# Performance work log

Hardware: AMD Instinct MI355X
Metric: run time of the kernel (lower is better)

Reference implementation:

```python
import jax, jax.numpy as jnp
import numpy as np

D_MODEL = 1024
NUM_HEADS = 16
D_K = D_MODEL // NUM_HEADS
THETA = 10000.0
BATCH, SEQ = 2, 2048


def _rope(xh, pos):
    # xh: (..., h, s, d_k), pos: (s,) int
    half = D_K // 2
    inv_freq = THETA ** (-jnp.arange(half, dtype=jnp.float32) * 2.0 / D_K)  # (half,)
    ang = pos.astype(jnp.float32)[:, None] * inv_freq[None, :]              # (s, half)
    cos, sin = jnp.cos(ang), jnp.sin(ang)
    x1 = xh[..., 0::2]  # (..., h, s, half)
    x2 = xh[..., 1::2]
    r1 = x1 * cos - x2 * sin
    r2 = x1 * sin + x2 * cos
    out = jnp.stack([r1, r2], axis=-1)            # (..., h, s, half, 2)
    return out.reshape(xh.shape)


def setup_inputs() -> dict:
    key = jax.random.key(0)
    k1, k2, k3 = jax.random.split(key, 3)
    scale_qkv = (6.0 / (3 * D_MODEL + D_MODEL)) ** 0.5  # xavier uniform bound
    scale_o = (6.0 / (2 * D_MODEL)) ** 0.5
    return {
        "x": jax.random.normal(k1, (BATCH, SEQ, D_MODEL), dtype=jnp.float32),
        "token_positions": jnp.arange(SEQ, dtype=jnp.int64 if jax.config.jax_enable_x64 else jnp.int32),
        "qkv_proj": jax.random.uniform(k2, (3 * D_MODEL, D_MODEL), jnp.float32, -scale_qkv, scale_qkv),
        "o_proj": jax.random.uniform(k3, (D_MODEL, D_MODEL), jnp.float32, -scale_o, scale_o),
    }


def reference(x, token_positions, qkv_proj, o_proj):
    # fused QKV projection: x @ qkv_proj^T
    qkv = jnp.einsum('bsd,ed->bse', x, qkv_proj)          # (b, s, 3*d_model)
    q, k, v = jnp.split(qkv, 3, axis=-1)

    def to_heads(t):
        b, s, _ = t.shape
        return t.reshape(b, s, NUM_HEADS, D_K).transpose(0, 2, 1, 3)  # (b, h, s, d_k)

    qh, kh, vh = to_heads(q), to_heads(k), to_heads(v)
    qh = _rope(qh, token_positions)
    kh = _rope(kh, token_positions)

    scores = jnp.einsum('bhqd,bhkd->bhqk', qh, kh) / (D_K ** 0.5)
    s = x.shape[-2]
    causal = jnp.tril(jnp.ones((s, s), dtype=bool))
    scores = jnp.where(causal, scores, -jnp.inf)
    attn = jax.nn.softmax(scores, axis=-1)
    out = jnp.einsum('bhqk,bhkd->bhqd', attn, vh)          # (b, h, s, d_k)
    out = out.transpose(0, 2, 1, 3).reshape(x.shape[0], s, D_MODEL)
    return jnp.einsum('bsd,od->bso', out, o_proj)
```

## Files before the change

### kernel.cpp

```cpp
#include <hip/hip_runtime.h>
#include <hip/hip_bf16.h>
#include <math.h>

typedef __bf16 bf16_t;
typedef __attribute__((ext_vector_type(2))) __bf16 bf16x2;
typedef __attribute__((ext_vector_type(4))) __bf16 bf16x4;
typedef __attribute__((ext_vector_type(8))) __bf16 bf16x8;
typedef __attribute__((ext_vector_type(4))) float f32x4;

#define BATCH  2
#define SEQ    2048
#define DMODEL 1024
#define NHEADS 16
#define DK     64

typedef const __attribute__((address_space(1))) void* gas_t;
typedef __attribute__((address_space(3))) void* las_t;

#define X_N (BATCH * SEQ * DMODEL)
#define W_N (3 * DMODEL * DMODEL)
#define O_N (DMODEL * DMODEL)

__global__ __launch_bounds__(256) void convert_kernel(
    const float* __restrict__ x, const float* __restrict__ w, const float* __restrict__ o,
    bf16_t* __restrict__ xb, bf16_t* __restrict__ wb, bf16_t* __restrict__ ob)
{
    const int gid = blockIdx.x * 256 + threadIdx.x;
    const float* src; bf16_t* dst; int base = gid * 8;
    if (base < X_N)                { src = x; dst = xb; }
    else if (base < X_N + W_N)     { src = w; dst = wb; base -= X_N; }
    else                           { src = o; dst = ob; base -= X_N + W_N; }
    const f32x4 lo = *(const f32x4*)(src + base);
    const f32x4 hi = *(const f32x4*)(src + base + 4);
    bf16x8 r;
    r[0] = (bf16_t)lo[0]; r[1] = (bf16_t)lo[1]; r[2] = (bf16_t)lo[2]; r[3] = (bf16_t)lo[3];
    r[4] = (bf16_t)hi[0]; r[5] = (bf16_t)hi[1]; r[6] = (bf16_t)hi[2]; r[7] = (bf16_t)hi[3];
    *(bf16x8*)(dst + base) = r;
}

__device__ __forceinline__ void gemm128_body(
    const bf16_t* __restrict__ A, const bf16_t* __restrict__ B,
    int rowBase, int colBase, bf16_t* ldsA, bf16_t* ldsB, f32x4 acc[4][4])
{
    const int tid  = threadIdx.x;
    const int lane = tid & 63;
    const int l15  = lane & 15, quad = lane >> 4;
    const int qr   = ((tid >> 6) >> 1) * 64;
    const int qc   = ((tid >> 6) & 1) * 64;

    const int c0 = tid, c1 = tid + 256;
    const int r0 = c0 >> 2, kc0 = (c0 & 3) * 8;
    const int r1 = c1 >> 2, kc1 = (c1 & 3) * 8;
    const bf16_t* ga0 = A + (size_t)(rowBase + r0) * DMODEL + kc0;
    const bf16_t* ga1 = A + (size_t)(rowBase + r1) * DMODEL + kc1;
    const bf16_t* gb0 = B + (size_t)(colBase + r0) * DMODEL + kc0;
    const bf16_t* gb1 = B + (size_t)(colBase + r1) * DMODEL + kc1;

    for (int k0 = 0; k0 < DMODEL; k0 += 32) {
        __syncthreads();
        __builtin_amdgcn_global_load_lds((gas_t)(ga0 + k0), (las_t)(ldsA + c0 * 8), 16, 0, 0);
        __builtin_amdgcn_global_load_lds((gas_t)(ga1 + k0), (las_t)(ldsA + c1 * 8), 16, 0, 0);
        __builtin_amdgcn_global_load_lds((gas_t)(gb0 + k0), (las_t)(ldsB + c0 * 8), 16, 0, 0);
        __builtin_amdgcn_global_load_lds((gas_t)(gb1 + k0), (las_t)(ldsB + c1 * 8), 16, 0, 0);
        __syncthreads();

        bf16x8 af[4], bfr[4];
#pragma unroll
        for (int i = 0; i < 4; ++i)
            af[i] = *(const bf16x8*)&ldsA[(qr + i * 16 + l15) * 32 + quad * 8];
#pragma unroll
        for (int j = 0; j < 4; ++j)
            bfr[j] = *(const bf16x8*)&ldsB[(qc + j * 16 + l15) * 32 + quad * 8];
#pragma unroll
        for (int i = 0; i < 4; ++i)
#pragma unroll
            for (int j = 0; j < 4; ++j)
                acc[i][j] = __builtin_amdgcn_mfma_f32_16x16x32_bf16(af[i], bfr[j], acc[i][j], 0, 0, 0);
    }
}

__global__ __launch_bounds__(256) void qkv_gemm_kernel(
    const bf16_t* __restrict__ x, const bf16_t* __restrict__ w,
    const int* __restrict__ pos,
    bf16_t* __restrict__ qo, bf16_t* __restrict__ ko, bf16_t* __restrict__ vt)
{
    __shared__ bf16_t ldsA[128 * 32];
    __shared__ bf16_t ldsB[128 * 32];
    const int bid = blockIdx.x;
    const int xcd = bid & 7, t = bid >> 3;
    const int xh  = xcd >> 2, yh = xcd & 3;
    const int bx  = xh * 12 + (t % 12);
    const int by  = yh * 8  + (t / 12);
    const int rowBase = by * 128;
    const int colBase = bx * 128;
    f32x4 acc[4][4] = {};
    gemm128_body(x, w, rowBase, colBase, ldsA, ldsB, acc);

    const int lane = threadIdx.x & 63;
    const int l15 = lane & 15, quad = lane >> 4;
    const int qr = ((threadIdx.x >> 6) >> 1) * 64;
    const int qc = ((threadIdx.x >> 6) & 1) * 64;
#pragma unroll
    for (int j = 0; j < 4; ++j) {
        const int col  = colBase + qc + j * 16 + l15;
        const int part = col >> 10;
        const int h    = (col & 1023) >> 6;
        const int d    = col & 63;
        bf16_t* op = (part == 0) ? qo : (part == 1) ? ko : vt;
        if (part < 2) {
            const float invf  = exp2f(-(float)(d >> 1) * 0.4152410118609203f);
            const float psign = (d & 1) ? 1.f : -1.f;
#pragma unroll
            for (int i = 0; i < 4; ++i) {
#pragma unroll
                for (int r = 0; r < 4; ++r) {
                    const int m = rowBase + qr + i * 16 + quad * 4 + r;
                    const int b = m >> 11;
                    const int s = m & (SEQ - 1);
                    const float ang = (float)pos[s] * invf;
                    const float sn_ = __sinf(ang);
                    const float c_  = __cosf(ang);
                    const float v = acc[i][j][r];
                    const float p = __shfl_xor(v, 1);
                    const float res = fmaf(p, psign * sn_, v * c_);
                    op[((size_t)(b * NHEADS + h) * SEQ + s) * DK + d] = (bf16_t)res;
                }
            }
        } else {
#pragma unroll
            for (int i = 0; i < 4; ++i) {
#pragma unroll
                for (int r = 0; r < 4; ++r) {
                    const int m = rowBase + qr + i * 16 + quad * 4 + r;
                    const int b = m >> 11;
                    const int s = m & (SEQ - 1);
                    const int sp = (s & ~63) | ((s & 15) << 2) | ((s >> 4) & 3);
                    op[(size_t)(b * NHEADS + h) * SEQ * DK + (size_t)d * SEQ + sp]
                        = (bf16_t)acc[i][j][r];
                }
            }
        }
    }
}

__global__ __launch_bounds__(256) void out_gemm_kernel(
    const bf16_t* __restrict__ a, const bf16_t* __restrict__ w, float* __restrict__ out)
{
    __shared__ bf16_t ldsA[2 * 128 * 64];
    __shared__ bf16_t ldsB[2 * 64 * 64];
    const int tid  = threadIdx.x;
    const int lane = tid & 63;
    const int l15  = lane & 15, quad = lane >> 4;
    const int l7   = l15 & 7;
    const int wv   = tid >> 6;
    const int bid = blockIdx.x;
    const int xcd = bid & 7, t = bid >> 3;
    const int xh  = xcd >> 2, yh = xcd & 3;
    const int bx  = xh * 8 + (t & 7);
    const int by  = yh * 8 + (t >> 3);
    const int rowBase = by * 128;
    const int colBase = bx * 64;

    const int sr   = tid >> 3;
    const int scol = ((tid & 7) ^ (sr & 7)) * 8;
    const bf16_t* ga = a + (size_t)(rowBase + sr) * DMODEL + scol;
    const bf16_t* gb = w + (size_t)(colBase + sr) * DMODEL + scol;
    const int dd = tid * 8;

#pragma unroll
    for (int u = 0; u < 4; ++u)
        __builtin_amdgcn_global_load_lds((gas_t)(ga + (size_t)u * 32 * DMODEL),
                                         (las_t)(ldsA + dd + u * 2048), 16, 0, 0);
#pragma unroll
    for (int u = 0; u < 2; ++u)
        __builtin_amdgcn_global_load_lds((gas_t)(gb + (size_t)u * 32 * DMODEL),
                                         (las_t)(ldsB + dd + u * 2048), 16, 0, 0);
    __syncthreads();

    f32x4 acc[2][4] = {};
    int buf = 0;
    for (int k0 = 0; k0 < DMODEL; k0 += 64) {
        if (k0 + 64 < DMODEL) {
            const int offA = (buf ^ 1) * 8192, offB = (buf ^ 1) * 4096;
#pragma unroll
            for (int u = 0; u < 4; ++u)
                __builtin_amdgcn_global_load_lds((gas_t)(ga + k0 + 64 + (size_t)u * 32 * DMODEL),
                                                 (las_t)(ldsA + offA + dd + u * 2048), 16, 0, 0);
#pragma unroll
            for (int u = 0; u < 2; ++u)
                __builtin_amdgcn_global_load_lds((gas_t)(gb + k0 + 64 + (size_t)u * 32 * DMODEL),
                                                 (las_t)(ldsB + offB + dd + u * 2048), 16, 0, 0);
        }
        const bf16_t* La = ldsA + buf * 8192;
        const bf16_t* Lb = ldsB + buf * 4096;
#pragma unroll
        for (int kk = 0; kk < 2; ++kk) {
            const int sw = ((kk * 4 + quad) ^ l7) * 8;
            bf16x8 af[2], bfr[4];
#pragma unroll
            for (int i = 0; i < 2; ++i)
                af[i] = *(const bf16x8*)&La[(wv * 32 + i * 16 + l15) * 64 + sw];
#pragma unroll
            for (int j = 0; j < 4; ++j)
                bfr[j] = *(const bf16x8*)&Lb[(j * 16 + l15) * 64 + sw];
#pragma unroll
            for (int i = 0; i < 2; ++i)
#pragma unroll
                for (int j = 0; j < 4; ++j)
                    acc[i][j] = __builtin_amdgcn_mfma_f32_16x16x32_bf16(af[i], bfr[j], acc[i][j], 0, 0, 0);
        }
        __syncthreads();
        buf ^= 1;
    }
#pragma unroll
    for (int i = 0; i < 2; ++i) {
#pragma unroll
        for (int r = 0; r < 4; ++r) {
            const int m = rowBase + wv * 32 + i * 16 + quad * 4 + r;
#pragma unroll
            for (int j = 0; j < 4; ++j)
                out[(size_t)m * DMODEL + colBase + j * 16 + l15] = acc[i][j][r];
        }
    }
}

__global__ __launch_bounds__(256) void attn_kernel(
    const bf16_t* __restrict__ Q, const bf16_t* __restrict__ K,
    const bf16_t* __restrict__ VT, bf16_t* __restrict__ AO)
{
    __shared__ bf16_t Kb[64 * 64];
    __shared__ bf16_t Vb[64 * 64];
    __shared__ bf16_t Pb[4][16 * 72];

    const int bh = blockIdx.x & 31;
    const int j  = blockIdx.x >> 5;
    const int lo = j & 7, hi = j >> 3;
    const int qb = (hi == 0) ? lo
                 : (hi == 1) ? (31 - lo)
                 : (hi == 2) ? (8 + lo)
                 :             (23 - lo);
    const int nt = qb + 1;

    const int tid  = threadIdx.x;
    const int wave = tid >> 6, lane = tid & 63;
    const int l15  = lane & 15, quad = lane >> 4;
    const int q0   = qb * 64 + wave * 16;
    const size_t hb = (size_t)bh * SEQ * DK;

    const int r0 = tid >> 3;
    const int sc = ((tid & 7) ^ (r0 & 7)) * 8;
    const int dd0 = tid * 8, dd1 = (tid + 256) * 8;

    bf16x8 aq0, aq1;
    {
        const bf16_t* qrow = Q + hb + (size_t)(q0 + l15) * DK + quad * 8;
        aq0 = *(const bf16x8*)qrow;
        aq1 = *(const bf16x8*)(qrow + 32);
#pragma unroll
        for (int i = 0; i < 8; ++i) {
            aq0[i] = (bf16_t)((float)aq0[i] * 0.125f);
            aq1[i] = (bf16_t)((float)aq1[i] * 0.125f);
        }
    }

    f32x4 oacc[4] = {};
    float lsum[4] = {};
    const int swA = (quad ^ (l15 & 7)) * 8;
    const int swB = ((4 + quad) ^ (l15 & 7)) * 8;

    for (int kb = 0; kb < nt; ++kb) {
        __syncthreads();
        {
            const bf16_t* kg = K  + hb + (size_t)kb * 64 * DK + (size_t)r0 * DK  + sc;
            const bf16_t* vg = VT + hb + kb * 64 + (size_t)r0 * SEQ + sc;
            __builtin_amdgcn_global_load_lds((gas_t)kg,              (las_t)(&Kb[dd0]), 16, 0, 0);
            __builtin_amdgcn_global_load_lds((gas_t)(kg + 32 * DK),  (las_t)(&Kb[dd1]), 16, 0, 0);
            __builtin_amdgcn_global_load_lds((gas_t)vg,              (las_t)(&Vb[dd0]), 16, 0, 0);
            __builtin_amdgcn_global_load_lds((gas_t)(vg + 32 * SEQ), (las_t)(&Vb[dd1]), 16, 0, 0);
        }
        __syncthreads();

        const bool nm = (kb == qb);

        bf16x8 kf0[4], kf1[4];
#pragma unroll
        for (int c = 0; c < 4; ++c) {
            kf0[c] = *(const bf16x8*)&Kb[(c * 16 + l15) * 64 + swA];
            kf1[c] = *(const bf16x8*)&Kb[(c * 16 + l15) * 64 + swB];
        }
        f32x4 sc4[4];
#pragma unroll
        for (int c = 0; c < 4; ++c) {
            f32x4 z = {};
            z = __builtin_amdgcn_mfma_f32_16x16x32_bf16(aq0, kf0[c], z, 0, 0, 0);
            z = __builtin_amdgcn_mfma_f32_16x16x32_bf16(aq1, kf1[c], z, 0, 0, 0);
            sc4[c] = z;
        }
#pragma unroll
        for (int r = 0; r < 4; ++r) {
            bf16x4 pr;
#pragma unroll
            for (int c = 0; c < 4; ++c) {
                float s = sc4[c][r];
                if (nm) {
                    const int key = kb * 64 + c * 16 + l15;
                    const int qa  = q0 + quad * 4 + r;
                    s = (key <= qa) ? s : -INFINITY;
                }
                const float p = __expf(s - 8.0f);
                lsum[r] += p;
                pr[c] = (bf16_t)p;
            }
            *(bf16x4*)&Pb[wave][(quad * 4 + r) * 72 + l15 * 4] = pr;
        }
        asm volatile("s_waitcnt lgkmcnt(0)" ::: "memory");

        const bf16x8 ap0 = *(const bf16x8*)&Pb[wave][l15 * 72 + quad * 8];
        const bf16x8 ap1 = *(const bf16x8*)&Pb[wave][l15 * 72 + 32 + quad * 8];
#pragma unroll
        for (int t = 0; t < 4; ++t) {
            const bf16x8 bv0 = *(const bf16x8*)&Vb[(t * 16 + l15) * 64 + swA];
            const bf16x8 bv1 = *(const bf16x8*)&Vb[(t * 16 + l15) * 64 + swB];
            oacc[t] = __builtin_amdgcn_mfma_f32_16x16x32_bf16(ap0, bv0, oacc[t], 0, 0, 0);
            oacc[t] = __builtin_amdgcn_mfma_f32_16x16x32_bf16(ap1, bv1, oacc[t], 0, 0, 0);
        }
    }

    const int b = bh >> 4, h = bh & 15;
    float inv[4];
#pragma unroll
    for (int r = 0; r < 4; ++r) {
        float s = lsum[r];
        s += __shfl_xor(s, 1);
        s += __shfl_xor(s, 2);
        s += __shfl_xor(s, 4);
        s += __shfl_xor(s, 8);
        inv[r] = 1.0f / s;
    }
#pragma unroll
    for (int t = 0; t < 4; ++t)
#pragma unroll
        for (int r = 0; r < 4; ++r) {
            const int qa = q0 + quad * 4 + r;
            AO[(size_t)(b * SEQ + qa) * DMODEL + h * 64 + t * 16 + l15] =
                (bf16_t)(oacc[t][r] * inv[r]);
        }
}

extern "C" void kernel_launch(void* const* d_in, const int* in_sizes, int n_in,
                              void* d_out, int out_size, void* d_ws, size_t ws_size,
                              hipStream_t stream) {
    (void)in_sizes; (void)n_in; (void)out_size; (void)ws_size;
    const float* x    = (const float*)d_in[0];
    const int*   pos  = (const int*)d_in[1];
    const float* qkvw = (const float*)d_in[2];
    const float* ow   = (const float*)d_in[3];
    float* out = (float*)d_out;

    const size_t HEAD_ELEMS = (size_t)BATCH * NHEADS * SEQ * DK;
    bf16_t* Qw  = (bf16_t*)d_ws;
    bf16_t* Kw  = Qw + HEAD_ELEMS;
    bf16_t* Vt  = Kw + HEAD_ELEMS;
    bf16_t* AO  = Vt + HEAD_ELEMS;
    bf16_t* xb  = AO;
    bf16_t* wb  = AO + X_N;
    bf16_t* ob  = wb + W_N;

    convert_kernel<<<dim3(4096), 256, 0, stream>>>(x, qkvw, ow, xb, wb, ob);
    qkv_gemm_kernel<<<dim3(768), 256, 0, stream>>>(xb, wb, pos, Qw, Kw, Vt);
    attn_kernel<<<dim3(1024), 256, 0, stream>>>(Qw, Kw, Vt, AO);
    out_gemm_kernel<<<dim3(512), 256, 0, stream>>>(AO, ob, out);
}
```

Baseline: 183.0 us.

## Rewrite QKV GEMM with 256x192 tiles, double-buffered LDS and swizzle

Replaces the 128x128, k=32, single-buffer QKV GEMM with a 512-thread block computing 256x192 tiles. It uses a 64-wide k step, a double-buffered LDS prefetch with explicit vmcnt waits, an XOR swizzle to avoid LDS bank conflicts, and setprio around the MFMA bursts. Larger tiles raise arithmetic intensity and cut global traffic, and the prefetch overlaps loads with compute. The trade-off is 256 blocks (one wave of CUs), heavy LDS use (~112KB) and more accumulator registers per thread, which lowers occupancy.

```diff
diff --git a/kernel.cpp b/kernel.cpp
--- a/kernel.cpp
+++ b/kernel.cpp
@@ -38,83 +38,105 @@
     *(bf16x8*)(dst + base) = r;
 }
 
-__device__ __forceinline__ void gemm128_body(
-    const bf16_t* __restrict__ A, const bf16_t* __restrict__ B,
-    int rowBase, int colBase, bf16_t* ldsA, bf16_t* ldsB, f32x4 acc[4][4])
-{
-    const int tid  = threadIdx.x;
-    const int lane = tid & 63;
-    const int l15  = lane & 15, quad = lane >> 4;
-    const int qr   = ((tid >> 6) >> 1) * 64;
-    const int qc   = ((tid >> 6) & 1) * 64;
-
-    const int c0 = tid, c1 = tid + 256;
-    const int r0 = c0 >> 2, kc0 = (c0 & 3) * 8;
-    const int r1 = c1 >> 2, kc1 = (c1 & 3) * 8;
-    const bf16_t* ga0 = A + (size_t)(rowBase + r0) * DMODEL + kc0;
-    const bf16_t* ga1 = A + (size_t)(rowBase + r1) * DMODEL + kc1;
-    const bf16_t* gb0 = B + (size_t)(colBase + r0) * DMODEL + kc0;
-    const bf16_t* gb1 = B + (size_t)(colBase + r1) * DMODEL + kc1;
-
-    for (int k0 = 0; k0 < DMODEL; k0 += 32) {
-        __syncthreads();
-        __builtin_amdgcn_global_load_lds((gas_t)(ga0 + k0), (las_t)(ldsA + c0 * 8), 16, 0, 0);
-        __builtin_amdgcn_global_load_lds((gas_t)(ga1 + k0), (las_t)(ldsA + c1 * 8), 16, 0, 0);
-        __builtin_amdgcn_global_load_lds((gas_t)(gb0 + k0), (las_t)(ldsB + c0 * 8), 16, 0, 0);
-        __builtin_amdgcn_global_load_lds((gas_t)(gb1 + k0), (las_t)(ldsB + c1 * 8), 16, 0, 0);
-        __syncthreads();
-
-        bf16x8 af[4], bfr[4];
-#pragma unroll
-        for (int i = 0; i < 4; ++i)
-            af[i] = *(const bf16x8*)&ldsA[(qr + i * 16 + l15) * 32 + quad * 8];
-#pragma unroll
-        for (int j = 0; j < 4; ++j)
-            bfr[j] = *(const bf16x8*)&ldsB[(qc + j * 16 + l15) * 32 + quad * 8];
-#pragma unroll
-        for (int i = 0; i < 4; ++i)
-#pragma unroll
-            for (int j = 0; j < 4; ++j)
-                acc[i][j] = __builtin_amdgcn_mfma_f32_16x16x32_bf16(af[i], bfr[j], acc[i][j], 0, 0, 0);
-    }
-}
-
-__global__ __launch_bounds__(256) void qkv_gemm_kernel(
+__global__ __launch_bounds__(512) void qkv_gemm_kernel(
     const bf16_t* __restrict__ x, const bf16_t* __restrict__ w,
     const int* __restrict__ pos,
     bf16_t* __restrict__ qo, bf16_t* __restrict__ ko, bf16_t* __restrict__ vt)
 {
-    __shared__ bf16_t ldsA[128 * 32];
-    __shared__ bf16_t ldsB[128 * 32];
+    __shared__ bf16_t Abuf[2][256 * 64];
+    __shared__ bf16_t Bbuf[2][192 * 64];
+
+    const int tid  = threadIdx.x;
+    const int lane = tid & 63;
+    const int l15  = lane & 15, quad = lane >> 4;
+    const int l7   = l15 & 7;
+    const int wv   = tid >> 6;
+    const int wr   = wv >> 2;
+    const int wc   = wv & 3;
+
     const int bid = blockIdx.x;
-    const int xcd = bid & 7, t = bid >> 3;
-    const int xh  = xcd >> 2, yh = xcd & 3;
-    const int bx  = xh * 12 + (t % 12);
-    const int by  = yh * 8  + (t / 12);
-    const int rowBase = by * 128;
-    const int colBase = bx * 128;
-    f32x4 acc[4][4] = {};
-    gemm128_body(x, w, rowBase, colBase, ldsA, ldsB, acc);
-
-    const int lane = threadIdx.x & 63;
-    const int l15 = lane & 15, quad = lane >> 4;
-    const int qr = ((threadIdx.x >> 6) >> 1) * 64;
-    const int qc = ((threadIdx.x >> 6) & 1) * 64;
-#pragma unroll
-    for (int j = 0; j < 4; ++j) {
-        const int col  = colBase + qc + j * 16 + l15;
-        const int part = col >> 10;
-        const int h    = (col & 1023) >> 6;
-        const int d    = col & 63;
+    const int xcd = bid & 7, tt = bid >> 3;
+    const int yh  = xcd >> 1, ch = xcd & 1;
+    const int bx  = ch * 8 + (tt & 7);
+    const int by  = yh * 4 + (tt >> 3);
+    const int rowBase = by * 256;
+    const int colBase = bx * 192;
+
+    const int r0   = tid >> 3;
+    const int scol = ((tid & 7) ^ (r0 & 7)) * 8;
+    const bf16_t* Ax = x + (size_t)(rowBase + r0) * DMODEL + scol;
+    const bf16_t* Bx = w + (size_t)(colBase + r0) * DMODEL + scol;
+
+    f32x4 acc[8][3] = {};
+
+#define STAGE(kt, bufi)                                                          \
+    {                                                                            \
+        const int k0_ = (kt) * 64;                                               \
+        _Pragma("unroll")                                                        \
+        for (int l = 0; l < 4; ++l)                                              \
+            __builtin_amdgcn_global_load_lds(                                    \
+                (gas_t)(Ax + (size_t)(l * 64) * DMODEL + k0_),                   \
+                (las_t)(&Abuf[bufi][(l * 512 + tid) * 8]), 16, 0, 0);            \
+        _Pragma("unroll")                                                        \
+        for (int l = 0; l < 3; ++l)                                              \
+            __builtin_amdgcn_global_load_lds(                                    \
+                (gas_t)(Bx + (size_t)(l * 64) * DMODEL + k0_),                   \
+                (las_t)(&Bbuf[bufi][(l * 512 + tid) * 8]), 16, 0, 0);            \
+    }
+
+    STAGE(0, 0)
+    STAGE(1, 1)
+    asm volatile("s_waitcnt vmcnt(7)" ::: "memory");
+    __builtin_amdgcn_s_barrier();
+    __builtin_amdgcn_sched_barrier(0);
+
+    for (int t = 0; t < 16; ++t) {
+        const int buf = t & 1;
+#pragma unroll
+        for (int kk = 0; kk < 2; ++kk) {
+            const int sw = ((kk * 4 + quad) ^ l7) * 8;
+            bf16x8 bfr[3];
+#pragma unroll
+            for (int j = 0; j < 3; ++j)
+                bfr[j] = *(const bf16x8*)&Bbuf[buf][(wc * 48 + j * 16 + l15) * 64 + sw];
+            __builtin_amdgcn_s_setprio(1);
+#pragma unroll
+            for (int i = 0; i < 8; ++i) {
+                const bf16x8 af = *(const bf16x8*)&Abuf[buf][(wr * 128 + i * 16 + l15) * 64 + sw];
+#pragma unroll
+                for (int j = 0; j < 3; ++j)
+                    acc[i][j] = __builtin_amdgcn_mfma_f32_16x16x32_bf16(af, bfr[j], acc[i][j], 0, 0, 0);
+            }
+            __builtin_amdgcn_s_setprio(0);
+        }
+        __builtin_amdgcn_s_barrier();
+        __builtin_amdgcn_sched_barrier(0);
+        if (t + 2 < 16) {
+            STAGE(t + 2, buf)
+            asm volatile("s_waitcnt vmcnt(7)" ::: "memory");
+        } else {
+            asm volatile("s_waitcnt vmcnt(0)" ::: "memory");
+        }
+        __builtin_amdgcn_s_barrier();
+        __builtin_amdgcn_sched_barrier(0);
+    }
+#undef STAGE
+
+#pragma unroll
+    for (int j = 0; j < 3; ++j) {
+        const int colj = colBase + wc * 48 + j * 16;
+        const int part = colj >> 10;
+        const int h    = (colj & 1023) >> 6;
+        const int d    = (colj & 63) + l15;
         bf16_t* op = (part == 0) ? qo : (part == 1) ? ko : vt;
         if (part < 2) {
             const float invf  = exp2f(-(float)(d >> 1) * 0.4152410118609203f);
             const float psign = (d & 1) ? 1.f : -1.f;
 #pragma unroll
-            for (int i = 0; i < 4; ++i) {
+            for (int i = 0; i < 8; ++i) {
 #pragma unroll
                 for (int r = 0; r < 4; ++r) {
-                    const int m = rowBase + qr + i * 16 + quad * 4 + r;
+                    const int m = rowBase + wr * 128 + i * 16 + quad * 4 + r;
                     const int b = m >> 11;
                     const int s = m & (SEQ - 1);
                     const float ang = (float)pos[s] * invf;
@@ -128,10 +150,10 @@
             }
         } else {
 #pragma unroll
-            for (int i = 0; i < 4; ++i) {
+            for (int i = 0; i < 8; ++i) {
 #pragma unroll
                 for (int r = 0; r < 4; ++r) {
-                    const int m = rowBase + qr + i * 16 + quad * 4 + r;
+                    const int m = rowBase + wr * 128 + i * 16 + quad * 4 + r;
                     const int b = m >> 11;
                     const int s = m & (SEQ - 1);
                     const int sp = (s & ~63) | ((s & 15) << 2) | ((s >> 4) & 3);
@@ -367,7 +389,7 @@
     bf16_t* ob  = wb + W_N;
 
     convert_kernel<<<dim3(4096), 256, 0, stream>>>(x, qkvw, ow, xb, wb, ob);
-    qkv_gemm_kernel<<<dim3(768), 256, 0, stream>>>(xb, wb, pos, Qw, Kw, Vt);
+    qkv_gemm_kernel<<<dim3(256), 512, 0, stream>>>(xb, wb, pos, Qw, Kw, Vt);
     attn_kernel<<<dim3(1024), 256, 0, stream>>>(Qw, Kw, Vt, AO);
     out_gemm_kernel<<<dim3(512), 256, 0, stream>>>(AO, ob, out);
 }
```

Result: faster. 172.2 us (-5.9%).
